# Kernel optimization log

Hardware: AMD Instinct MI355X
Metric: run time of the kernel (lower is better)

## Reference

```python
import jax, jax.numpy as jnp
import numpy as np

# ---- hyperparameters matching init_kwargs / input_specs ----
K = 16          # max neighbors kept per node (avg degree)
ALPHA = 0.5     # FGW trade-off (POT default used in the repo)
FW_ITERS = 5    # Frank-Wolfe (conditional-gradient) outer iterations
SK_ITERS = 20   # log-domain Sinkhorn inner iterations
REG = 0.1       # entropic regularization for the inner OT solve
NEG = -1e9      # "log(0)" for masked (padded) neighborhood slots


def build_neighbors(edge_index, n, k):
    """Fixed-size (padded) neighbor table from a COO edge list."""
    src, dst = edge_index[0], edge_index[1]
    order = jnp.argsort(src)
    s_src, s_dst = src[order], dst[order]
    ids = jnp.arange(n)
    start = jnp.searchsorted(s_src, ids)
    end = jnp.searchsorted(s_src, ids, side='right')
    cnt = jnp.minimum(end - start, k)                       # [n]
    pos = start[:, None] + jnp.arange(k)[None, :]           # [n,k]
    valid = jnp.arange(k)[None, :] < cnt[:, None]           # [n,k]
    nbrs = s_dst[jnp.clip(pos, 0, s_src.shape[0] - 1)]      # [n,k]
    return nbrs, valid


def reference(x, edge_index, templates, templates_features):
    n, d = x.shape
    nbrs, valid = build_neighbors(edge_index, n, K)
    # local node set per node: self + up to K neighbors -> K1 = K+1 slots
    S = jnp.concatenate([jnp.arange(n)[:, None], nbrs], axis=1)            # [n,K1]
    mask = jnp.concatenate([jnp.ones((n, 1), bool), valid], axis=1)        # [n,K1]
    mf = mask.astype(x.dtype)

    # local subgraph adjacency: A[i,a,b] = 1 iff edge S[i,a] -> S[i,b]
    nbrs_of = nbrs[S]                                                      # [n,K1,K]
    valid_of = valid[S]
    eq = (nbrs_of[:, :, None, :] == S[:, None, :, None]) & valid_of[:, :, None, :]
    C1 = eq.any(-1).astype(x.dtype) * mf[:, :, None] * mf[:, None, :]      # [n,K1,K1]

    F1 = x[S] * mf[:, :, None]                                             # [n,K1,d]
    F2 = templates_features                                                # [T,t,d]
    # squared-euclidean feature cost M[i,T,a,b] = ||F1[i,a]-F2[T,b]||^2
    M = (jnp.sum(F1 ** 2, -1)[:, None, :, None]
         + jnp.sum(F2 ** 2, -1)[None, :, None, :]
         - 2.0 * jnp.einsum('nad,tbd->ntab', F1, F2))                      # [n,T,K1,t]

    cnt1 = mf.sum(1)                                                       # [n] (>=1: self)
    p = mf / cnt1[:, None]                                                 # [n,K1] uniform masked
    t_n = templates.shape[1]
    q = jnp.full((t_n,), 1.0 / t_n, x.dtype)
    C2 = templates                                                         # [T,t,t]

    # GW square-loss decomposition (POT): tens = constC - 2*C1 @ T @ C2^T
    constC = (jnp.einsum('nab,nb->na', C1 ** 2, p)[:, None, :, None]
              + jnp.einsum('tab,b->ta', C2 ** 2, q)[None, :, None, :])     # [n,T,K1,t]

    def tens_of(T):
        tmp = jnp.einsum('nac,ntcd->ntad', C1, T)
        cross = jnp.einsum('ntad,tbd->ntab', tmp, C2)
        return constC - 2.0 * cross

    logp = jnp.where(mask, -jnp.log(cnt1)[:, None], NEG)[:, None, :]       # [n,1,K1]
    logq = -jnp.log(jnp.asarray(t_n, x.dtype))                             # scalar

    def sinkhorn(G):
        logK = -G / REG                                                    # [n,T,K1,t]
        f = jnp.zeros(G.shape[:3], G.dtype)
        g = jnp.zeros(G.shape[:2] + (t_n,), G.dtype)
        def body(_, fg):
            f, g = fg
            g = logq - jax.nn.logsumexp(logK + f[..., :, None], axis=-2)
            f = logp - jax.nn.logsumexp(logK + g[..., None, :], axis=-1)
            return (f, g)
        f, g = jax.lax.fori_loop(0, SK_ITERS, body, (f, g))
        return jnp.exp(f[..., :, None] + g[..., None, :] + logK)

    T0 = p[:, None, :, None] * q[None, None, None, :]                      # [n,1->T,K1,t]
    T0 = jnp.broadcast_to(T0, M.shape)

    def fw_step(T, k):
        tens = tens_of(T)
        G = (1.0 - ALPHA) * M + 2.0 * ALPHA * tens                         # FGW gradient
        Tn = sinkhorn(G)                                                   # linear-min oracle
        gamma = 2.0 / (k + 2.0)
        return (1.0 - gamma) * T + gamma * Tn, None

    T, _ = jax.lax.scan(fw_step, T0, jnp.arange(FW_ITERS, dtype=x.dtype))

    tens = tens_of(T)
    dist = ((1.0 - ALPHA) * jnp.sum(M * T, axis=(-2, -1))
            + ALPHA * jnp.sum(tens * T, axis=(-2, -1)))                    # [n,T]
    return dist


def setup_inputs() -> dict:
    key = jax.random.key(0)
    k1, k2, k3, k4 = jax.random.split(key, 4)
    n, d, e = 10000, 128, 160000
    n_T, t_n = 10, 10
    x = jax.random.normal(k1, (n, d), jnp.float32)
    edge_index = jax.random.randint(k2, (2, e), 0, n, jnp.int64)
    templates = jax.random.uniform(k3, (n_T, t_n, t_n), jnp.float32)
    templates_features = jax.random.normal(k4, (n_T, t_n, d), jnp.float32)
    return {"x": x, "edge_index": edge_index,
            "templates": templates, "templates_features": templates_features}
```

## Files before the change

kernel.cpp:

```cpp
#include <hip/hip_runtime.h>
#include <math.h>

#define NNODE 10000
#define NEDGE 160000
#define KNB   16
#define K1    17
#define NT    10
#define TN    10
#define DF    128
#define CAP   64
#define NEG_BIG (-1e9f)

#define LOGQ2      (-3.32192809489f)
#define KB_SCALE   (-14.4269504089f)
#define CR_SCALE   (28.8539008178f)
#define G_SCALE    (-0.069314718056f)
#define LN2        0.69314718056f
#define TINYF      1e-30f

#if defined(__has_builtin)
#if __has_builtin(__builtin_amdgcn_exp2f)
#define EXP2F(x) __builtin_amdgcn_exp2f(x)
#endif
#if __has_builtin(__builtin_amdgcn_rcpf)
#define RCPF(x) __builtin_amdgcn_rcpf(x)
#endif
#endif
#ifndef EXP2F
#define EXP2F(x) __expf((x) * LN2)
#endif
#ifndef RCPF
#define RCPF(x) (1.0f / (x))
#endif
#define LOG2F(x) __log2f(x)

#define CBAR() asm volatile("" ::: "memory")

__device__ __forceinline__ float2 pk_add(float2 a, float2 b) { return make_float2(a.x + b.x, a.y + b.y); }
__device__ __forceinline__ float2 pk_sub(float2 a, float2 b) { return make_float2(a.x - b.x, a.y - b.y); }
__device__ __forceinline__ float2 pk_mul(float2 a, float2 b) { return make_float2(a.x * b.x, a.y * b.y); }
__device__ __forceinline__ float2 pk_max(float2 a, float2 b) { return make_float2(fmaxf(a.x, b.x), fmaxf(a.y, b.y)); }
__device__ __forceinline__ float2 pk_fma(float2 a, float2 b, float2 c) { return make_float2(fmaf(a.x, b.x, c.x), fmaf(a.y, b.y, c.y)); }
__device__ __forceinline__ float2 pk_exp2(float2 a) { return make_float2(EXP2F(a.x), EXP2F(a.y)); }
__device__ __forceinline__ float clamp120(float x) { return fminf(120.f, fmaxf(-120.f, x)); }

__device__ __forceinline__ int detect_wide_wave(const int* ei) {
  int z = 0;
  if ((threadIdx.x & 63) == 0) {
#pragma unroll
    for (int i = 0; i < 32; ++i) z |= ei[2 * i + 1];
  }
  z = __shfl(z, 0, 64);
  return z == 0;
}

__global__ void __launch_bounds__(256) k_prep(const int* __restrict__ ei,
                                              int* cnt, int* ebuf,
                                              const float* __restrict__ x,
                                              const float* __restrict__ tf,
                                              const float* __restrict__ tmpl,
                                              float* __restrict__ dots,
                                              float* __restrict__ nxv,
                                              float* __restrict__ nF2,
                                              float* __restrict__ Bq) {
  __shared__ float xs[16][DF];
  const int tid = threadIdx.x;
  if (blockIdx.x < 625) {
    int wide = detect_wide_wave(ei);
    int e = blockIdx.x * 256 + tid;
    int s = wide ? ei[2 * e] : ei[e];
    int pos = atomicAdd(&cnt[s], 1);
    if (pos < CAP) ebuf[s * CAP + pos] = e;
    return;
  }
  const int db = blockIdx.x - 625;
  if (db == 0 && tid < NT * TN) {
    const float* fp = tf + (size_t)tid * DF;
    float s = 0.f;
    for (int d = 0; d < DF; ++d) { float v = fp[d]; s += v * v; }
    nF2[tid] = s;
    const float* cp = tmpl + (size_t)tid * TN;
    float s2 = 0.f;
    for (int c = 0; c < TN; ++c) { float v = cp[c]; s2 += v * v; }
    Bq[tid] = 0.1f * s2;
  }
  const int nb = db * 16;
  const int nvalid = (NNODE - nb) < 16 ? (NNODE - nb) : 16;
  {
    const float4* xg = (const float4*)(x + (size_t)nb * DF);
    float4* xl = (float4*)&xs[0][0];
    for (int i = tid; i < nvalid * (DF / 4); i += 256) xl[i] = xg[i];
  }
  __syncthreads();
  for (int o = tid; o < nvalid * (NT * TN); o += 256) {
    int n = o / (NT * TN);
    int tb = o - n * (NT * TN);
    const float4* fp = (const float4*)(tf + (size_t)tb * DF);
    const float4* xp = (const float4*)&xs[n][0];
    float s = 0.f;
#pragma unroll
    for (int d = 0; d < DF / 4; ++d) {
      float4 a = xp[d], f = fp[d];
      s += a.x * f.x + a.y * f.y + a.z * f.z + a.w * f.w;
    }
    dots[(size_t)(nb + n) * (NT * TN) + tb] = s;
  }
  if (tid < nvalid) {
    const float4* xp = (const float4*)&xs[tid][0];
    float s = 0.f;
#pragma unroll
    for (int d = 0; d < DF / 4; ++d) {
      float4 a = xp[d];
      s += a.x * a.x + a.y * a.y + a.z * a.z + a.w * a.w;
    }
    nxv[nb + tid] = s;
  }
}

__global__ void __launch_bounds__(256) k_select(const int* __restrict__ ei,
                                                const int* __restrict__ cnt,
                                                const int* __restrict__ ebuf,
                                                int* __restrict__ nbrs,
                                                int* __restrict__ kcnt,
                                                int* __restrict__ Sg) {
  const int wv = threadIdx.x >> 6;
  const int lane = threadIdx.x & 63;
  const int i = blockIdx.x * 4 + wv;
  if (i >= NNODE) return;
  const int wide = detect_wide_wave(ei);
  int c = cnt[i]; c = c > CAP ? CAP : c;
  int v = (lane < c) ? ebuf[i * CAP + lane] : 0x7FFFFFFF;
#pragma unroll
  for (int k = 2; k <= 64; k <<= 1) {
#pragma unroll
    for (int j = k >> 1; j > 0; j >>= 1) {
      int pv = __shfl_xor(v, j, 64);
      bool up = ((lane & k) == 0);
      bool lower = ((lane & j) == 0);
      int mn = v < pv ? v : pv;
      int mx = v < pv ? pv : v;
      v = (lower == up) ? mn : mx;
    }
  }
  const int m = c < KNB ? c : KNB;
  if (lane == 0) { kcnt[i] = m; Sg[i * K1] = i; }
  if (lane < KNB) {
    int d = 0;
    if (lane < m) d = wide ? ei[2 * (NEDGE + v)] : ei[NEDGE + v];
    nbrs[i * KNB + lane] = d;
    Sg[i * K1 + 1 + lane] = d;
  }
}

__global__ void __launch_bounds__(256) k_c1b(const int* __restrict__ nbrs,
                                             const int* __restrict__ kcnt,
                                             const int* __restrict__ Sg,
                                             unsigned int* __restrict__ bitsG,
                                             float* __restrict__ Ag) {
  int idx = blockIdx.x * 256 + threadIdx.x;
  if (idx >= NNODE * K1) return;
  int i = idx / K1;
  int a = idx - i * K1;
  int kc = kcnt[i];
  unsigned int vmask = (kc >= KNB) ? 0x1FFFFu : ((2u << kc) - 1u);
  unsigned int bits = 0;
  bool va = (a == 0) || (a - 1 < kc);
  if (va) {
    int S[K1];
#pragma unroll
    for (int b = 0; b < K1; ++b) S[b] = Sg[i * K1 + b];
    int u = S[a];
    int ku = kcnt[u];
    const int* np = nbrs + (size_t)u * KNB;
    for (int j = 0; j < ku; ++j) {
      int w = np[j];
#pragma unroll
      for (int b = 0; b < K1; ++b) bits |= (S[b] == w) ? (1u << b) : 0u;
    }
    bits &= vmask;
  }
  bitsG[idx] = bits;
  Ag[idx] = (float)__popc(bits) / (float)(1 + kc);
}

__global__ void __launch_bounds__(128, 3) k_main(
    const float* __restrict__ tmpl,
    const int* __restrict__ kcnt, const int* __restrict__ Sg,
    const unsigned int* __restrict__ bitsG, const float* __restrict__ Ag,
    const float* __restrict__ dots, const float* __restrict__ nxv,
    const float* __restrict__ nF2, const float* __restrict__ Bq,
    float* __restrict__ out)
{
  __shared__ float KT[2 * 6 * 204 + 48];
  __shared__ float fL[2][6][20];
  __shared__ float gL[2][6][12];
  __shared__ float uL[2][6][20];
  __shared__ float wL[2][6][12];
  __shared__ float accL[2][6][TN];

  const int wv = threadIdx.x >> 6;
  const int lane = threadIdx.x & 63;
  const int p0 = lane / 10;
  const int b = lane - p0 * 10;
  const bool act = (p0 < 5);
  const int p = act ? p0 : 5;
  const int node = blockIdx.x;
  const int tb = act ? ((wv * 5 + p0) * TN + b) : 0;
  float* KTp = &KT[(wv * 6 + p) * 204];

  const int kc = kcnt[node];
  const float cnt1 = (float)(1 + kc);
  const float inv_cnt1 = 1.f / cnt1;
  const float logp2v = -LOG2F(cnt1);
  const float lp2_r0 = ((b == 0) || (b - 1 < kc)) ? logp2v : NEG_BIG;
  const float lp2_r1 = ((9 + b) < kc) ? logp2v : NEG_BIG;

  float2 c2v[5];
  {
    const float2* cp = (const float2*)(tmpl + (size_t)tb * TN);
#pragma unroll
    for (int j = 0; j < 5; ++j) c2v[j] = cp[j];
  }
  const float Bb = Bq[tb];
  const float nf2b = nF2[tb];

  float2 Kb2v[8]; float kb16;
  float2 Tp2[10];
#pragma unroll
  for (int j = 0; j < 10; ++j) Tp2[j] = make_float2(0.f, 0.f);
  unsigned int bw[K1];
#pragma unroll
  for (int a = 0; a < K1; ++a) {
    bool va = (a == 0) || (a - 1 < kc);
    int sa = Sg[node * K1 + a];
    float Ma = (va ? (nxv[sa] - 2.f * dots[(size_t)sa * (NT * TN) + tb]) : 0.f) + nf2b;
    float base = 0.5f * Ma + Ag[node * K1 + a] + Bb;
    float kv = KB_SCALE * base;
    float tv = va ? (inv_cnt1 * 0.1f) : 0.f;
    if (a == 16) kb16 = kv;
    else if (a & 1) Kb2v[a >> 1].y = kv;
    else Kb2v[a >> 1].x = kv;
    if (a < 10) Tp2[a].x = tv; else Tp2[a - 10].y = tv;
    bw[a] = bitsG[node * K1 + a];
  }

  float2 Kc2v[8]; float k16 = 0.f;
  float2 Kr0v[5], Kr1v[5];
  float2 gr[5];
  float g2 = 0.f, fr0 = 0.f, fr1 = 0.f;

#pragma unroll 1
  for (int k = 0; k < 6; ++k) {
#pragma unroll
    for (int a = 0; a < K1; ++a)
      KTp[a * 12 + b] = (a < 10) ? Tp2[a].x : Tp2[a - 10].y;
    CBAR();
    float R[K1];
#pragma unroll
    for (int c = 0; c < K1; ++c) {
      const float* row = &KTp[c * 12];
      float4 u0 = *(const float4*)row;
      float4 u1 = *(const float4*)(row + 4);
      float2 u2 = *(const float2*)(row + 8);
      float2 accA = pk_mul(make_float2(u0.x, u0.y), c2v[0]);
      accA = pk_fma(make_float2(u0.z, u0.w), c2v[1], accA);
      float2 accB = pk_mul(make_float2(u1.x, u1.y), c2v[2]);
      accB = pk_fma(make_float2(u1.z, u1.w), c2v[3], accB);
      accA = pk_fma(u2, c2v[4], accA);
      accA = pk_add(accA, accB);
      R[c] = accA.x + accA.y;
    }
#pragma unroll
    for (int a = 0; a < K1; ++a) {
      float cr = 0.f;
      unsigned int m = bw[a];
      if (m) {
#pragma unroll
        for (int c = 0; c < K1; ++c)
          if (m & (1u << c)) cr += R[c];
      }
      float base = (a == 16) ? kb16 : ((a & 1) ? Kb2v[a >> 1].y : Kb2v[a >> 1].x);
      float val = base + CR_SCALE * cr;
      if (a == 16) k16 = val;
      else if (a & 1) Kc2v[a >> 1].y = val;
      else Kc2v[a >> 1].x = val;
    }

    if (k == 5) {
      float acc = 0.f;
#pragma unroll
      for (int a = 0; a < K1; ++a) {
        bool va = (a == 0) || (a - 1 < kc);
        int sa = Sg[node * K1 + a];
        float Ma = (va ? (nxv[sa] - 2.f * dots[(size_t)sa * (NT * TN) + tb]) : 0.f) + nf2b;
        float kcv = (a == 16) ? k16 : ((a & 1) ? Kc2v[a >> 1].y : Kc2v[a >> 1].x);
        float tpv = (a < 10) ? Tp2[a].x : Tp2[a - 10].y;
        acc += tpv * (0.25f * Ma + 0.5f * (G_SCALE * kcv));
      }
      accL[wv][p][b] = acc;
      CBAR();
      if (lane < 5) {
        float s = 0.f;
#pragma unroll
        for (int j = 0; j < TN; ++j) s += accL[wv][lane][j];
        out[node * NT + wv * 5 + lane] = s;
      }
      return;
    }

    CBAR();
#pragma unroll
    for (int a = 0; a < 16; ++a) KTp[a * 12 + b] = (a & 1) ? Kc2v[a >> 1].y : Kc2v[a >> 1].x;
    KTp[16 * 12 + b] = k16;
    CBAR();
    {
      const float* r0 = &KTp[b * 12];
      float4 u0 = *(const float4*)r0;
      float4 u1 = *(const float4*)(r0 + 4);
      float2 u2 = *(const float2*)(r0 + 8);
      Kr0v[0] = make_float2(u0.x, u0.y); Kr0v[1] = make_float2(u0.z, u0.w);
      Kr0v[2] = make_float2(u1.x, u1.y); Kr0v[3] = make_float2(u1.z, u1.w);
      Kr0v[4] = u2;
      const float* r1 = &KTp[(10 + b) * 12];
      float4 w0 = *(const float4*)r1;
      float4 w1 = *(const float4*)(r1 + 4);
      float2 w2 = *(const float2*)(r1 + 8);
      Kr1v[0] = make_float2(w0.x, w0.y); Kr1v[1] = make_float2(w0.z, w0.w);
      Kr1v[2] = make_float2(w1.x, w1.y); Kr1v[3] = make_float2(w1.z, w1.w);
      Kr1v[4] = w2;
    }

#pragma unroll 1
    for (int it = 0; it < 2; ++it) {
      float2 v[8]; float v16;
      if (it == 0) {
#pragma unroll
        for (int i = 0; i < 8; ++i) v[i] = Kc2v[i];
        v16 = k16;
      } else {
        float4 f0 = *(const float4*)&fL[wv][p][0];
        float4 f1 = *(const float4*)&fL[wv][p][4];
        float4 f2 = *(const float4*)&fL[wv][p][8];
        float4 f3 = *(const float4*)&fL[wv][p][12];
        float fx = fL[wv][p][16];
        v[0] = pk_add(Kc2v[0], make_float2(f0.x, f0.y));
        v[1] = pk_add(Kc2v[1], make_float2(f0.z, f0.w));
        v[2] = pk_add(Kc2v[2], make_float2(f1.x, f1.y));
        v[3] = pk_add(Kc2v[3], make_float2(f1.z, f1.w));
        v[4] = pk_add(Kc2v[4], make_float2(f2.x, f2.y));
        v[5] = pk_add(Kc2v[5], make_float2(f2.z, f2.w));
        v[6] = pk_add(Kc2v[6], make_float2(f3.x, f3.y));
        v[7] = pk_add(Kc2v[7], make_float2(f3.z, f3.w));
        v16 = k16 + fx;
      }
      float2 m01 = pk_max(pk_max(v[0], v[1]), pk_max(v[2], v[3]));
      float2 m23 = pk_max(pk_max(v[4], v[5]), pk_max(v[6], v[7]));
      float2 mm = pk_max(m01, m23);
      float mx = fmaxf(fmaxf(mm.x, mm.y), v16);
      float2 mxb = make_float2(mx, mx);
      float2 ssA = pk_exp2(pk_sub(v[0], mxb));
      ssA = pk_add(ssA, pk_exp2(pk_sub(v[1], mxb)));
      ssA = pk_add(ssA, pk_exp2(pk_sub(v[2], mxb)));
      ssA = pk_add(ssA, pk_exp2(pk_sub(v[3], mxb)));
      float2 ssB = pk_exp2(pk_sub(v[4], mxb));
      ssB = pk_add(ssB, pk_exp2(pk_sub(v[5], mxb)));
      ssB = pk_add(ssB, pk_exp2(pk_sub(v[6], mxb)));
      ssB = pk_add(ssB, pk_exp2(pk_sub(v[7], mxb)));
      float2 ss = pk_add(ssA, ssB);
      float s = ss.x + ss.y + EXP2F(v16 - mx);
      g2 = LOGQ2 - mx - LOG2F(s);
      gL[wv][p][b] = g2;
      CBAR();
      {
        float4 g0 = *(const float4*)&gL[wv][p][0];
        float4 g1 = *(const float4*)&gL[wv][p][4];
        float2 gx = *(const float2*)&gL[wv][p][8];
        gr[0] = make_float2(g0.x, g0.y); gr[1] = make_float2(g0.z, g0.w);
        gr[2] = make_float2(g1.x, g1.y); gr[3] = make_float2(g1.z, g1.w);
        gr[4] = gx;
      }
      float2 w0[5], w1[5];
#pragma unroll
      for (int j = 0; j < 5; ++j) w0[j] = pk_add(Kr0v[j], gr[j]);
#pragma unroll
      for (int j = 0; j < 5; ++j) w1[j] = pk_add(Kr1v[j], gr[j]);
      float2 a01 = pk_max(pk_max(w0[0], w0[1]), pk_max(w0[2], w0[3]));
      a01 = pk_max(a01, w0[4]);
      float mxa = fmaxf(a01.x, a01.y);
      float2 b01 = pk_max(pk_max(w1[0], w1[1]), pk_max(w1[2], w1[3]));
      b01 = pk_max(b01, w1[4]);
      float mxb2 = fmaxf(b01.x, b01.y);
      float2 mab = make_float2(mxa, mxa);
      float2 mbb = make_float2(mxb2, mxb2);
      float2 sx = pk_exp2(pk_sub(w0[0], mab));
      sx = pk_add(sx, pk_exp2(pk_sub(w0[1], mab)));
      sx = pk_add(sx, pk_exp2(pk_sub(w0[2], mab)));
      sx = pk_add(sx, pk_exp2(pk_sub(w0[3], mab)));
      sx = pk_add(sx, pk_exp2(pk_sub(w0[4], mab)));
      float2 sy = pk_exp2(pk_sub(w1[0], mbb));
      sy = pk_add(sy, pk_exp2(pk_sub(w1[1], mbb)));
      sy = pk_add(sy, pk_exp2(pk_sub(w1[2], mbb)));
      sy = pk_add(sy, pk_exp2(pk_sub(w1[3], mbb)));
      sy = pk_add(sy, pk_exp2(pk_sub(w1[4], mbb)));
      fr0 = lp2_r0 - mxa - LOG2F(sx.x + sx.y);
      fr1 = lp2_r1 - mxb2 - LOG2F(sy.x + sy.y);
      fL[wv][p][b] = fr0;
      fL[wv][p][10 + b] = fr1;
      CBAR();
    }

    float2 Kcs2[10];
    float P00, P01, Q0;
    float2 Krs01[10];
    {
      float4 F0 = *(const float4*)&fL[wv][p][0];
      float4 F1 = *(const float4*)&fL[wv][p][4];
      float4 F2 = *(const float4*)&fL[wv][p][8];
      float4 F3 = *(const float4*)&fL[wv][p][12];
      float f16v = fL[wv][p][16];
      float fs[K1];
      fs[0] = F0.x; fs[1] = F0.y; fs[2] = F0.z; fs[3] = F0.w;
      fs[4] = F1.x; fs[5] = F1.y; fs[6] = F1.z; fs[7] = F1.w;
      fs[8] = F2.x; fs[9] = F2.y; fs[10] = F2.z; fs[11] = F2.w;
      fs[12] = F3.x; fs[13] = F3.y; fs[14] = F3.z; fs[15] = F3.w;
      fs[16] = f16v;
      float qs[K1];
#pragma unroll
      for (int a = 0; a < K1; ++a) {
        float kcv = (a == 16) ? k16 : ((a & 1) ? Kc2v[a >> 1].y : Kc2v[a >> 1].x);
        qs[a] = kcv + fs[a];
      }
      float sigma = qs[0];
#pragma unroll
      for (int a = 1; a < K1; ++a) sigma = fmaxf(sigma, qs[a]);
#pragma unroll
      for (int j = 0; j < 10; ++j) {
        float kx = EXP2F(qs[j] - sigma);
        float ky = (j < 7) ? EXP2F(qs[10 + j] - sigma) : 0.f;
        Kcs2[j] = make_float2(kx, ky);
      }
      Q0 = EXP2F(clamp120(LOGQ2 - sigma - g2));
      float2 a0[5], a1[5];
#pragma unroll
      for (int j = 0; j < 5; ++j) a0[j] = pk_add(Kr0v[j], gr[j]);
#pragma unroll
      for (int j = 0; j < 5; ++j) a1[j] = pk_add(Kr1v[j], gr[j]);
      float2 r0m = pk_max(pk_max(a0[0], a0[1]), pk_max(a0[2], a0[3]));
      r0m = pk_max(r0m, a0[4]);
      float rho0 = fmaxf(r0m.x, r0m.y);
      float2 r1m = pk_max(pk_max(a1[0], a1[1]), pk_max(a1[2], a1[3]));
      r1m = pk_max(r1m, a1[4]);
      float rho1 = fmaxf(r1m.x, r1m.y);
#pragma unroll
      for (int j = 0; j < 5; ++j) {
        Krs01[2 * j]     = make_float2(EXP2F(a0[j].x - rho0), EXP2F(a1[j].x - rho1));
        Krs01[2 * j + 1] = make_float2(EXP2F(a0[j].y - rho0), EXP2F(a1[j].y - rho1));
      }
      P00 = EXP2F(clamp120((lp2_r0 - rho0) - fr0));
      P01 = EXP2F(clamp120((lp2_r1 - rho1) - fr1));
    }

    float Slast, t0, t1;
    {
      float2 SA = pk_add(pk_add(Kcs2[0], Kcs2[1]), pk_add(Kcs2[2], Kcs2[3]));
      float2 SB = pk_add(pk_add(Kcs2[4], Kcs2[5]), pk_add(Kcs2[6], Kcs2[7]));
      float2 S2 = pk_add(pk_add(SA, SB), pk_add(Kcs2[8], Kcs2[9]));
      float S = fmaxf(S2.x + S2.y, TINYF);
      Slast = S;
      float wb = Q0 * RCPF(S);
      wL[wv][p][b] = wb;
      CBAR();
      float4 W0 = *(const float4*)&wL[wv][p][0];
      float4 W1 = *(const float4*)&wL[wv][p][4];
      float2 W2 = *(const float2*)&wL[wv][p][8];
      float2 tA = pk_mul(Krs01[0], make_float2(W0.x, W0.x));
      tA = pk_fma(Krs01[1], make_float2(W0.y, W0.y), tA);
      tA = pk_fma(Krs01[2], make_float2(W0.z, W0.z), tA);
      tA = pk_fma(Krs01[3], make_float2(W0.w, W0.w), tA);
      tA = pk_fma(Krs01[4], make_float2(W1.x, W1.x), tA);
      float2 tB = pk_mul(Krs01[5], make_float2(W1.y, W1.y));
      tB = pk_fma(Krs01[6], make_float2(W1.z, W1.z), tB);
      tB = pk_fma(Krs01[7], make_float2(W1.w, W1.w), tB);
      tB = pk_fma(Krs01[8], make_float2(W2.x, W2.x), tB);
      tB = pk_fma(Krs01[9], make_float2(W2.y, W2.y), tB);
      float2 t01 = pk_add(tA, tB);
      t0 = t01.x; t1 = t01.y;
    }
#pragma unroll 1
    for (int it = 0; it < 17; ++it) {
      float u0 = P00 * RCPF(fmaxf(t0, TINYF));
      float u1 = P01 * RCPF(fmaxf(t1, TINYF));
      *(float2*)&uL[wv][p][2 * b] = make_float2(u0, u1);
      CBAR();
      float4 U0 = *(const float4*)&uL[wv][p][0];
      float4 U1 = *(const float4*)&uL[wv][p][4];
      float4 U2 = *(const float4*)&uL[wv][p][8];
      float4 U3 = *(const float4*)&uL[wv][p][12];
      float4 U4 = *(const float4*)&uL[wv][p][16];
      float2 SA = pk_mul(Kcs2[0], make_float2(U0.x, U0.y));
      SA = pk_fma(Kcs2[1], make_float2(U0.z, U0.w), SA);
      SA = pk_fma(Kcs2[2], make_float2(U1.x, U1.y), SA);
      SA = pk_fma(Kcs2[3], make_float2(U1.z, U1.w), SA);
      SA = pk_fma(Kcs2[4], make_float2(U2.x, U2.y), SA);
      float2 SB = pk_mul(Kcs2[5], make_float2(U2.z, U2.w));
      SB = pk_fma(Kcs2[6], make_float2(U3.x, U3.y), SB);
      SB = pk_fma(Kcs2[7], make_float2(U3.z, U3.w), SB);
      SB = pk_fma(Kcs2[8], make_float2(U4.x, U4.y), SB);
      SB = pk_fma(Kcs2[9], make_float2(U4.z, U4.w), SB);
      float2 S2 = pk_add(SA, SB);
      float S = fmaxf(S2.x + S2.y, TINYF);
      Slast = S;
      float wb = Q0 * RCPF(S);
      wL[wv][p][b] = wb;
      CBAR();
      float4 W0 = *(const float4*)&wL[wv][p][0];
      float4 W1 = *(const float4*)&wL[wv][p][4];
      float2 W2 = *(const float2*)&wL[wv][p][8];
      float2 tA = pk_mul(Krs01[0], make_float2(W0.x, W0.x));
      tA = pk_fma(Krs01[1], make_float2(W0.y, W0.y), tA);
      tA = pk_fma(Krs01[2], make_float2(W0.z, W0.z), tA);
      tA = pk_fma(Krs01[3], make_float2(W0.w, W0.w), tA);
      tA = pk_fma(Krs01[4], make_float2(W1.x, W1.x), tA);
      float2 tB = pk_mul(Krs01[5], make_float2(W1.y, W1.y));
      tB = pk_fma(Krs01[6], make_float2(W1.z, W1.z), tB);
      tB = pk_fma(Krs01[7], make_float2(W1.w, W1.w), tB);
      tB = pk_fma(Krs01[8], make_float2(W2.x, W2.x), tB);
      tB = pk_fma(Krs01[9], make_float2(W2.y, W2.y), tB);
      float2 t01 = pk_add(tA, tB);
      t0 = t01.x; t1 = t01.y;
    }

    {
      float u0 = P00 * RCPF(fmaxf(t0, TINYF));
      float u1 = P01 * RCPF(fmaxf(t1, TINYF));
      *(float2*)&uL[wv][p][2 * b] = make_float2(u0, u1);
      CBAR();
      float4 U0 = *(const float4*)&uL[wv][p][0];
      float4 U1 = *(const float4*)&uL[wv][p][4];
      float4 U2 = *(const float4*)&uL[wv][p][8];
      float4 U3 = *(const float4*)&uL[wv][p][12];
      float4 U4 = *(const float4*)&uL[wv][p][16];
      const float gam = 2.f / ((float)k + 2.f);
      const float gs = gam * 0.1f * RCPF(Slast);
      const float om = 1.f - gam;
      const float2 omb = make_float2(om, om);
      const float2 gsb = make_float2(gs, gs);
      float2 uu[10];
      uu[0] = make_float2(U0.x, U0.y); uu[1] = make_float2(U0.z, U0.w);
      uu[2] = make_float2(U1.x, U1.y); uu[3] = make_float2(U1.z, U1.w);
      uu[4] = make_float2(U2.x, U2.y); uu[5] = make_float2(U2.z, U2.w);
      uu[6] = make_float2(U3.x, U3.y); uu[7] = make_float2(U3.z, U3.w);
      uu[8] = make_float2(U4.x, U4.y); uu[9] = make_float2(U4.z, U4.w);
#pragma unroll
      for (int j = 0; j < 10; ++j)
        Tp2[j] = pk_fma(omb, Tp2[j], pk_mul(gsb, pk_mul(Kcs2[j], uu[j])));
    }
  }
}

extern "C" void kernel_launch(void* const* d_in, const int* in_sizes, int n_in,
                              void* d_out, int out_size, void* d_ws, size_t ws_size,
                              hipStream_t stream) {
  const float* x    = (const float*)d_in[0];
  const int*   ei   = (const int*)d_in[1];
  const float* tmpl = (const float*)d_in[2];
  const float* tf   = (const float*)d_in[3];
  float* out = (float*)d_out;

  int* cnt  = (int*)d_ws;
  int* ebuf = cnt + NNODE;
  int* nbrs = ebuf + (size_t)NNODE * CAP;
  int* kcnt = nbrs + (size_t)NNODE * KNB;
  int* Sg   = kcnt + NNODE;
  unsigned int* bits = (unsigned int*)(Sg + (size_t)NNODE * K1);
  float* Ag   = (float*)(bits + (size_t)NNODE * K1);
  float* dots = Ag + (size_t)NNODE * K1;
  float* nxv  = dots + (size_t)NNODE * (NT * TN);
  float* nF2  = nxv + NNODE;
  float* Bq   = nF2 + NT * TN;

  hipMemsetAsync(cnt, 0, NNODE * sizeof(int), stream);
  k_prep<<<625 + (NNODE + 15) / 16, 256, 0, stream>>>(ei, cnt, ebuf, x, tf, tmpl,
                                                      dots, nxv, nF2, Bq);
  k_select<<<(NNODE + 3) / 4, 256, 0, stream>>>(ei, cnt, ebuf, nbrs, kcnt, Sg);
  k_c1b<<<(NNODE * K1 + 255) / 256, 256, 0, stream>>>(nbrs, kcnt, Sg, bits, Ag);
  k_main<<<NNODE, 128, 0, stream>>>(tmpl, kcnt, Sg, bits, Ag, dots, nxv, nF2, Bq, out);
}
```

Measured before the change: 540.4 us.

## Pack six (node,template) pairs per wavefront instead of five per node

Work is re-indexed from one block per node with five templates per wavefront to a flat list of (node,template) pairs, with six pairs per 64-lane wavefront (60 active lanes instead of 50). The launch uses fewer blocks and makes fuller use of each wavefront's lanes. Shared scratch arrays are aliased into the per-pair KT region to keep LDS footprint small. P01 is zeroed for lanes beyond the 17 rows. Lanes in one wavefront may now belong to different nodes, so per-node loads are less uniform.

```diff
diff --git a/kernel.cpp b/kernel.cpp
--- a/kernel.cpp
+++ b/kernel.cpp
@@ -9,6 +9,7 @@
 #define TN    10
 #define DF    128
 #define CAP   64
+#define NPAIR (NNODE * NT)
 #define NEG_BIG (-1e9f)
 
 #define LOGQ2      (-3.32192809489f)
@@ -191,22 +192,25 @@
     const float* __restrict__ nF2, const float* __restrict__ Bq,
     float* __restrict__ out)
 {
-  __shared__ float KT[2 * 6 * 204 + 48];
-  __shared__ float fL[2][6][20];
-  __shared__ float gL[2][6][12];
-  __shared__ float uL[2][6][20];
-  __shared__ float wL[2][6][12];
-  __shared__ float accL[2][6][TN];
+  __shared__ float SH[2 * 7 * 204 + 16];
 
   const int wv = threadIdx.x >> 6;
   const int lane = threadIdx.x & 63;
   const int p0 = lane / 10;
   const int b = lane - p0 * 10;
-  const bool act = (p0 < 5);
-  const int p = act ? p0 : 5;
-  const int node = blockIdx.x;
-  const int tb = act ? ((wv * 5 + p0) * TN + b) : 0;
-  float* KTp = &KT[(wv * 6 + p) * 204];
+  const int pairRaw = blockIdx.x * 12 + wv * 6 + p0;
+  const bool act = (p0 < 6) && (pairRaw < NPAIR);
+  const int pair = act ? pairRaw : 0;
+  const int node = pair / 10;
+  const int tI = pair - node * 10;
+  const int tb = tI * TN + b;
+
+  float* const KTp  = &SH[(wv * 7 + p0) * 204];
+  float* const fLp  = KTp;
+  float* const gLp  = KTp + 20;
+  float* const uLp  = KTp;
+  float* const wLp  = KTp + 20;
+  float* const accp = KTp + 32;
 
   const int kc = kcnt[node];
   const float cnt1 = (float)(1 + kc);
@@ -297,13 +301,13 @@
         float tpv = (a < 10) ? Tp2[a].x : Tp2[a - 10].y;
         acc += tpv * (0.25f * Ma + 0.5f * (G_SCALE * kcv));
       }
-      accL[wv][p][b] = acc;
-      CBAR();
-      if (lane < 5) {
+      accp[b] = acc;
+      CBAR();
+      if (act && b == 0) {
         float s = 0.f;
 #pragma unroll
-        for (int j = 0; j < TN; ++j) s += accL[wv][lane][j];
-        out[node * NT + wv * 5 + lane] = s;
+        for (int j = 0; j < TN; ++j) s += accp[j];
+        out[node * NT + tI] = s;
       }
       return;
     }
@@ -338,11 +342,11 @@
         for (int i = 0; i < 8; ++i) v[i] = Kc2v[i];
         v16 = k16;
       } else {
-        float4 f0 = *(const float4*)&fL[wv][p][0];
-        float4 f1 = *(const float4*)&fL[wv][p][4];
-        float4 f2 = *(const float4*)&fL[wv][p][8];
-        float4 f3 = *(const float4*)&fL[wv][p][12];
-        float fx = fL[wv][p][16];
+        float4 f0 = *(const float4*)&fLp[0];
+        float4 f1 = *(const float4*)&fLp[4];
+        float4 f2 = *(const float4*)&fLp[8];
+        float4 f3 = *(const float4*)&fLp[12];
+        float fx = fLp[16];
         v[0] = pk_add(Kc2v[0], make_float2(f0.x, f0.y));
         v[1] = pk_add(Kc2v[1], make_float2(f0.z, f0.w));
         v[2] = pk_add(Kc2v[2], make_float2(f1.x, f1.y));
@@ -369,12 +373,12 @@
       float2 ss = pk_add(ssA, ssB);
       float s = ss.x + ss.y + EXP2F(v16 - mx);
       g2 = LOGQ2 - mx - LOG2F(s);
-      gL[wv][p][b] = g2;
+      gLp[b] = g2;
       CBAR();
       {
-        float4 g0 = *(const float4*)&gL[wv][p][0];
-        float4 g1 = *(const float4*)&gL[wv][p][4];
-        float2 gx = *(const float2*)&gL[wv][p][8];
+        float4 g0 = *(const float4*)&gLp[0];
+        float4 g1 = *(const float4*)&gLp[4];
+        float2 gx = *(const float2*)&gLp[8];
         gr[0] = make_float2(g0.x, g0.y); gr[1] = make_float2(g0.z, g0.w);
         gr[2] = make_float2(g1.x, g1.y); gr[3] = make_float2(g1.z, g1.w);
         gr[4] = gx;
@@ -404,8 +408,8 @@
       sy = pk_add(sy, pk_exp2(pk_sub(w1[4], mbb)));
       fr0 = lp2_r0 - mxa - LOG2F(sx.x + sx.y);
       fr1 = lp2_r1 - mxb2 - LOG2F(sy.x + sy.y);
-      fL[wv][p][b] = fr0;
-      fL[wv][p][10 + b] = fr1;
+      fLp[b] = fr0;
+      fLp[10 + b] = fr1;
       CBAR();
     }
 
@@ -413,11 +417,11 @@
     float P00, P01, Q0;
     float2 Krs01[10];
     {
-      float4 F0 = *(const float4*)&fL[wv][p][0];
-      float4 F1 = *(const float4*)&fL[wv][p][4];
-      float4 F2 = *(const float4*)&fL[wv][p][8];
-      float4 F3 = *(const float4*)&fL[wv][p][12];
-      float f16v = fL[wv][p][16];
+      float4 F0 = *(const float4*)&fLp[0];
+      float4 F1 = *(const float4*)&fLp[4];
+      float4 F2 = *(const float4*)&fLp[8];
+      float4 F3 = *(const float4*)&fLp[12];
+      float f16v = fLp[16];
       float fs[K1];
       fs[0] = F0.x; fs[1] = F0.y; fs[2] = F0.z; fs[3] = F0.w;
       fs[4] = F1.x; fs[5] = F1.y; fs[6] = F1.z; fs[7] = F1.w;
@@ -457,7 +461,7 @@
         Krs01[2 * j + 1] = make_float2(EXP2F(a0[j].y - rho0), EXP2F(a1[j].y - rho1));
       }
       P00 = EXP2F(clamp120((lp2_r0 - rho0) - fr0));
-      P01 = EXP2F(clamp120((lp2_r1 - rho1) - fr1));
+      P01 = (b < 7) ? EXP2F(clamp120((lp2_r1 - rho1) - fr1)) : 0.f;
     }
 
     float Slast, t0, t1;
@@ -468,11 +472,11 @@
       float S = fmaxf(S2.x + S2.y, TINYF);
       Slast = S;
       float wb = Q0 * RCPF(S);
-      wL[wv][p][b] = wb;
-      CBAR();
-      float4 W0 = *(const float4*)&wL[wv][p][0];
-      float4 W1 = *(const float4*)&wL[wv][p][4];
-      float2 W2 = *(const float2*)&wL[wv][p][8];
+      wLp[b] = wb;
+      CBAR();
+      float4 W0 = *(const float4*)&wLp[0];
+      float4 W1 = *(const float4*)&wLp[4];
+      float2 W2 = *(const float2*)&wLp[8];
       float2 tA = pk_mul(Krs01[0], make_float2(W0.x, W0.x));
       tA = pk_fma(Krs01[1], make_float2(W0.y, W0.y), tA);
       tA = pk_fma(Krs01[2], make_float2(W0.z, W0.z), tA);
@@ -490,13 +494,13 @@
     for (int it = 0; it < 17; ++it) {
       float u0 = P00 * RCPF(fmaxf(t0, TINYF));
       float u1 = P01 * RCPF(fmaxf(t1, TINYF));
-      *(float2*)&uL[wv][p][2 * b] = make_float2(u0, u1);
-      CBAR();
-      float4 U0 = *(const float4*)&uL[wv][p][0];
-      float4 U1 = *(const float4*)&uL[wv][p][4];
-      float4 U2 = *(const float4*)&uL[wv][p][8];
-      float4 U3 = *(const float4*)&uL[wv][p][12];
-      float4 U4 = *(const float4*)&uL[wv][p][16];
+      *(float2*)&uLp[2 * b] = make_float2(u0, u1);
+      CBAR();
+      float4 U0 = *(const float4*)&uLp[0];
+      float4 U1 = *(const float4*)&uLp[4];
+      float4 U2 = *(const float4*)&uLp[8];
+      float4 U3 = *(const float4*)&uLp[12];
+      float4 U4 = *(const float4*)&uLp[16];
       float2 SA = pk_mul(Kcs2[0], make_float2(U0.x, U0.y));
       SA = pk_fma(Kcs2[1], make_float2(U0.z, U0.w), SA);
       SA = pk_fma(Kcs2[2], make_float2(U1.x, U1.y), SA);
@@ -511,11 +515,11 @@
       float S = fmaxf(S2.x + S2.y, TINYF);
       Slast = S;
       float wb = Q0 * RCPF(S);
-      wL[wv][p][b] = wb;
-      CBAR();
-      float4 W0 = *(const float4*)&wL[wv][p][0];
-      float4 W1 = *(const float4*)&wL[wv][p][4];
-      float2 W2 = *(const float2*)&wL[wv][p][8];
+      wLp[b] = wb;
+      CBAR();
+      float4 W0 = *(const float4*)&wLp[0];
+      float4 W1 = *(const float4*)&wLp[4];
+      float2 W2 = *(const float2*)&wLp[8];
       float2 tA = pk_mul(Krs01[0], make_float2(W0.x, W0.x));
       tA = pk_fma(Krs01[1], make_float2(W0.y, W0.y), tA);
       tA = pk_fma(Krs01[2], make_float2(W0.z, W0.z), tA);
@@ -533,13 +537,13 @@
     {
       float u0 = P00 * RCPF(fmaxf(t0, TINYF));
       float u1 = P01 * RCPF(fmaxf(t1, TINYF));
-      *(float2*)&uL[wv][p][2 * b] = make_float2(u0, u1);
-      CBAR();
-      float4 U0 = *(const float4*)&uL[wv][p][0];
-      float4 U1 = *(const float4*)&uL[wv][p][4];
-      float4 U2 = *(const float4*)&uL[wv][p][8];
-      float4 U3 = *(const float4*)&uL[wv][p][12];
-      float4 U4 = *(const float4*)&uL[wv][p][16];
+      *(float2*)&uLp[2 * b] = make_float2(u0, u1);
+      CBAR();
+      float4 U0 = *(const float4*)&uLp[0];
+      float4 U1 = *(const float4*)&uLp[4];
+      float4 U2 = *(const float4*)&uLp[8];
+      float4 U3 = *(const float4*)&uLp[12];
+      float4 U4 = *(const float4*)&uLp[16];
       const float gam = 2.f / ((float)k + 2.f);
       const float gs = gam * 0.1f * RCPF(Slast);
       const float om = 1.f - gam;
@@ -584,5 +588,5 @@
                                                       dots, nxv, nF2, Bq);
   k_select<<<(NNODE + 3) / 4, 256, 0, stream>>>(ei, cnt, ebuf, nbrs, kcnt, Sg);
   k_c1b<<<(NNODE * K1 + 255) / 256, 256, 0, stream>>>(nbrs, kcnt, Sg, bits, Ag);
-  k_main<<<NNODE, 128, 0, stream>>>(tmpl, kcnt, Sg, bits, Ag, dots, nxv, nF2, Bq, out);
+  k_main<<<(NPAIR + 11) / 12, 128, 0, stream>>>(tmpl, kcnt, Sg, bits, Ag, dots, nxv, nF2, Bq, out);
 }
```

Result: faster. 521.1 us (-3.6%).
